# Optimization experiments

Measured on AMD Instinct MI355X. Metric: run time of the kernel, lower is better.

Reference implementation:

```python
import jax, jax.numpy as jnp
import numpy as np

B, S, D = 8, 1024, 768
H = 12
HD = D // H
DROPOUT_P = 0.5


def setup_inputs() -> dict:
    key = jax.random.key(0)
    ks = jax.random.split(key, 9)
    scale = 1.0 / np.sqrt(D)
    return {
        "x": jax.random.normal(ks[0], (B, S, D), dtype=jnp.float32),
        "wq": jax.random.normal(ks[1], (D, D), dtype=jnp.float32) * scale,
        "bq": jax.random.normal(ks[2], (D,), dtype=jnp.float32) * 0.01,
        "wk": jax.random.normal(ks[3], (D, D), dtype=jnp.float32) * scale,
        "bk": jax.random.normal(ks[4], (D,), dtype=jnp.float32) * 0.01,
        "wv": jax.random.normal(ks[5], (D, D), dtype=jnp.float32) * scale,
        "bv": jax.random.normal(ks[6], (D,), dtype=jnp.float32) * 0.01,
        "wo": jax.random.normal(ks[7], (D, D), dtype=jnp.float32) * scale,
        "bo": jax.random.normal(ks[8], (D,), dtype=jnp.float32) * 0.01,
    }


def reference(x, wq, bq, wk, bk, wv, bv, wo, bo):
    # QKV projections (torch Linear: y = x @ W.T + b)
    def proj(w, b):
        y = jnp.einsum("bsd,ed->bse", x, w) + b
        # [B,S,D] -> [B,H,S,HD]
        return y.reshape(B, S, H, HD).transpose(0, 2, 1, 3)

    q = proj(wq, bq)
    k = proj(wk, bk)
    v = proj(wv, bv)

    scores = jnp.einsum("bhqd,bhkd->bhqk", q, k) / jnp.sqrt(
        jnp.asarray(HD, dtype=x.dtype)
    )
    # dropout BEFORE softmax (non-standard, faithful to source), training=True
    dkey = jax.random.key(42)
    keep = jax.random.bernoulli(dkey, 1.0 - DROPOUT_P, scores.shape)
    scores = jnp.where(keep, scores / (1.0 - DROPOUT_P), 0.0)

    attn = jax.nn.softmax(scores, axis=-1)
    o = jnp.einsum("bhqk,bhkd->bhqd", attn, v)
    o = o.transpose(0, 2, 1, 3).reshape(B, S, D)
    return jnp.einsum("bsd,ed->bse", o, wo) + bo
```

## Files before the change

### kernel.cpp

```cpp
#include <hip/hip_runtime.h>
#include <hip/hip_bf16.h>
#include <stdint.h>

typedef __bf16 bf16_t;
typedef __attribute__((ext_vector_type(8))) __bf16 bf16x8;
typedef __attribute__((ext_vector_type(4))) __bf16 bf16x4;
typedef __attribute__((ext_vector_type(4))) float f32x4;

#define MFMA16(a, b, c) __builtin_amdgcn_mfma_f32_16x16x32_bf16(a, b, c, 0, 0, 0)


__device__ __forceinline__ uint32_t rotl32(uint32_t v, uint32_t r) {
    return (v << r) | (v >> (32u - r));
}
__device__ __forceinline__ uint32_t tf_fold(uint32_t x0, uint32_t x1) {
    const uint32_t ks0 = 0u, ks1 = 42u, ks2 = 0x1BD11BDAu ^ 42u;
    x0 += ks0; x1 += ks1;
#define TF_R(r) { x0 += x1; x1 = rotl32(x1, r); x1 ^= x0; }
    TF_R(13) TF_R(15) TF_R(26) TF_R(6)   x0 += ks1; x1 += ks2 + 1u;
    TF_R(17) TF_R(29) TF_R(16) TF_R(24)  x0 += ks2; x1 += ks0 + 2u;
    TF_R(13) TF_R(15) TF_R(26) TF_R(6)   x0 += ks0; x1 += ks1 + 3u;
    TF_R(17) TF_R(29) TF_R(16) TF_R(24)  x0 += ks1; x1 += ks2 + 4u;
    TF_R(13) TF_R(15) TF_R(26) TF_R(6)   x0 += ks2; x1 += ks0 + 5u;
#undef TF_R
    return x0 ^ x1;
}

__device__ __forceinline__ bf16x8 cvt8(float4 a, float4 b) {
    bf16x8 v;
    v[0] = (bf16_t)a.x; v[1] = (bf16_t)a.y; v[2] = (bf16_t)a.z; v[3] = (bf16_t)a.w;
    v[4] = (bf16_t)b.x; v[5] = (bf16_t)b.y; v[6] = (bf16_t)b.z; v[7] = (bf16_t)b.w;
    return v;
}

__global__ __launch_bounds__(256, 2)
void qkv_gemm(const float* __restrict__ x,
              const float* __restrict__ wq, const float* __restrict__ bq,
              const float* __restrict__ wk, const float* __restrict__ bk,
              const float* __restrict__ wv, const float* __restrict__ bv,
              bf16_t* __restrict__ qb, bf16_t* __restrict__ kb, bf16_t* __restrict__ vtb)
{
    const int mt = blockIdx.x;
    const int nt = blockIdx.y;
    const int mat = blockIdx.z;
    const float* w   = (mat == 0) ? wq : ((mat == 1) ? wk : wv);
    const float* bia = (mat == 0) ? bq : ((mat == 1) ? bk : bv);

    __shared__ bf16_t As[128][40];
    __shared__ bf16_t Bs[128][40];

    const int t = threadIdx.x;
    const int wid = t >> 6, l = t & 63, l15 = l & 15, lg = l >> 4;
    const int wr = wid >> 1, wc = wid & 1;

    f32x4 acc[4][4] = {};

    const int srow = t >> 1, scol = (t & 1) * 16;
    const float* xa = x + (size_t)(mt * 128 + srow) * 768 + scol;
    const float* wa = w + (size_t)(nt * 128 + srow) * 768 + scol;

    for (int kt = 0; kt < 24; ++kt) {
        const float* pa = xa + kt * 32;
        const float* pb = wa + kt * 32;
        float4 a0 = *(const float4*)(pa + 0),  a1 = *(const float4*)(pa + 4);
        float4 a2 = *(const float4*)(pa + 8),  a3 = *(const float4*)(pa + 12);
        float4 b0 = *(const float4*)(pb + 0),  b1 = *(const float4*)(pb + 4);
        float4 b2 = *(const float4*)(pb + 8),  b3 = *(const float4*)(pb + 12);
        __syncthreads();
        *(bf16x8*)&As[srow][scol]     = cvt8(a0, a1);
        *(bf16x8*)&As[srow][scol + 8] = cvt8(a2, a3);
        *(bf16x8*)&Bs[srow][scol]     = cvt8(b0, b1);
        *(bf16x8*)&Bs[srow][scol + 8] = cvt8(b2, b3);
        __syncthreads();

        bf16x8 af[4], bf[4];
#pragma unroll
        for (int m = 0; m < 4; ++m) af[m] = *(const bf16x8*)&As[wr * 64 + m * 16 + l15][lg * 8];
#pragma unroll
        for (int n = 0; n < 4; ++n) bf[n] = *(const bf16x8*)&Bs[wc * 64 + n * 16 + l15][lg * 8];
#pragma unroll
        for (int m = 0; m < 4; ++m)
#pragma unroll
            for (int n = 0; n < 4; ++n)
                acc[m][n] = MFMA16(af[m], bf[n], acc[m][n]);
    }

    const int eb = nt * 128 + wc * 64;
    const int mb = mt * 128 + wr * 64;
#pragma unroll
    for (int n = 0; n < 4; ++n) {
        const int e = eb + n * 16 + l15;
        const float bias = bia[e];
        const int h = e >> 6, hd = e & 63;
#pragma unroll
        for (int m = 0; m < 4; ++m) {
            const int m0 = mb + m * 16 + lg * 4;
            const int b = m0 >> 10, s0 = m0 & 1023;
            if (mat == 2) {
                bf16x4 pv;
#pragma unroll
                for (int r = 0; r < 4; ++r) pv[r] = (bf16_t)(acc[m][n][r] + bias);
                *(bf16x4*)(vtb + (((size_t)(b * 12 + h)) << 16) + ((size_t)hd << 10) + s0) = pv;
            } else {
                bf16_t* dst = (mat == 0) ? qb : kb;
                const float sc = (mat == 0) ? 0.125f : 1.0f;
                const size_t base = (((size_t)(b * 12 + h)) << 16) + ((size_t)s0 << 6) + hd;
#pragma unroll
                for (int r = 0; r < 4; ++r)
                    dst[base + (size_t)r * 64] = (bf16_t)((acc[m][n][r] + bias) * sc);
            }
        }
    }
}

__global__ __launch_bounds__(256, 2)
void attn_kernel(const bf16_t* __restrict__ qb, const bf16_t* __restrict__ kb,
                 const bf16_t* __restrict__ vtb, bf16_t* __restrict__ ob)
{
    const int qt = blockIdx.x;
    const int bh = blockIdx.y;
    const int t = threadIdx.x, w = t >> 6, l = t & 63, l15 = l & 15, lg = l >> 4;

    __shared__ bf16_t Kl[64][72];
    __shared__ bf16_t Vl[64][72];
    __shared__ bf16_t Pl[4][16][72];

    const size_t base = ((size_t)bh) << 16;
    const int q0 = qt * 64 + w * 16;

    bf16x8 qf[2];
    {
        const size_t qbase = base + (size_t)(q0 + l15) * 64 + lg * 8;
        qf[0] = *(const bf16x8*)(qb + qbase);
        qf[1] = *(const bf16x8*)(qb + qbase + 32);
    }

    f32x4 oacc[4] = {};
    float mst[4], lst[4];
#pragma unroll
    for (int r = 0; r < 4; ++r) { mst[r] = -1e30f; lst[r] = 0.f; }

    const uint32_t fbase = ((uint32_t)bh) << 20;

    for (int kt = 0; kt < 16; ++kt) {
#pragma unroll
        for (int sdx = 0; sdx < 2; ++sdx) {
            const int idx = sdx * 256 + t;
            const int row = idx >> 3, seg = idx & 7;
            *(uint4*)&Kl[row][seg * 8] =
                *(const uint4*)(kb + base + ((size_t)(kt * 64 + row) << 6) + seg * 8);
            *(uint4*)&Vl[row][seg * 8] =
                *(const uint4*)(vtb + base + ((size_t)row << 10) + kt * 64 + seg * 8);
        }
        __syncthreads();

        f32x4 sc[4] = {};
#pragma unroll
        for (int ks = 0; ks < 2; ++ks)
#pragma unroll
            for (int n = 0; n < 4; ++n) {
                bf16x8 kf = *(const bf16x8*)&Kl[n * 16 + l15][ks * 32 + lg * 8];
                sc[n] = MFMA16(qf[ks], kf, sc[n]);
            }

#pragma unroll
        for (int n = 0; n < 4; ++n) {
            const uint32_t kg = (uint32_t)(kt * 64 + n * 16 + l15);
#pragma unroll
            for (int r = 0; r < 4; ++r) {
                const uint32_t f = fbase + ((uint32_t)(q0 + lg * 4 + r) << 10) + kg;
                const uint32_t bits = tf_fold(0u, f);
                sc[n][r] = (bits >> 31) ? 0.f : sc[n][r] * 2.f;
            }
        }

#pragma unroll
        for (int r = 0; r < 4; ++r) {
            float tm = fmaxf(fmaxf(sc[0][r], sc[1][r]), fmaxf(sc[2][r], sc[3][r]));
#pragma unroll
            for (int mk = 1; mk < 16; mk <<= 1) tm = fmaxf(tm, __shfl_xor(tm, mk));
            const float mnew = fmaxf(mst[r], tm);
            const float corr = __expf(mst[r] - mnew);
            float ps = 0.f;
#pragma unroll
            for (int n = 0; n < 4; ++n) {
                const float p = __expf(sc[n][r] - mnew);
                ps += p;
                Pl[w][lg * 4 + r][n * 16 + l15] = (bf16_t)p;
            }
#pragma unroll
            for (int mk = 1; mk < 16; mk <<= 1) ps += __shfl_xor(ps, mk);
            lst[r] = lst[r] * corr + ps;
            mst[r] = mnew;
#pragma unroll
            for (int n = 0; n < 4; ++n) oacc[n][r] *= corr;
        }

        {
            const bf16x8 pa0 = *(const bf16x8*)&Pl[w][l15][lg * 8];
            const bf16x8 pa1 = *(const bf16x8*)&Pl[w][l15][32 + lg * 8];
#pragma unroll
            for (int n = 0; n < 4; ++n) {
                const bf16x8 v0 = *(const bf16x8*)&Vl[n * 16 + l15][lg * 8];
                const bf16x8 v1 = *(const bf16x8*)&Vl[n * 16 + l15][32 + lg * 8];
                oacc[n] = MFMA16(pa0, v0, oacc[n]);
                oacc[n] = MFMA16(pa1, v1, oacc[n]);
            }
        }
        __syncthreads();
    }

    const int b = bh / 12, h = bh % 12;
#pragma unroll
    for (int r = 0; r < 4; ++r) {
        const float inv = 1.f / lst[r];
        const size_t row = ((size_t)(b * 1024 + q0 + lg * 4 + r)) * 768 + h * 64;
#pragma unroll
        for (int n = 0; n < 4; ++n)
            ob[row + n * 16 + l15] = (bf16_t)(oacc[n][r] * inv);
    }
}

__global__ __launch_bounds__(256, 2)
void out_gemm(const bf16_t* __restrict__ ob, const float* __restrict__ wo,
              const float* __restrict__ bo, float* __restrict__ out)
{
    const int mt = blockIdx.x, nt = blockIdx.y;
    __shared__ bf16_t As[128][40];
    __shared__ bf16_t Bs[128][40];
    const int t = threadIdx.x;
    const int wid = t >> 6, l = t & 63, l15 = l & 15, lg = l >> 4;
    const int wr = wid >> 1, wc = wid & 1;
    f32x4 acc[4][4] = {};

    const int srow = t >> 1, scol = (t & 1) * 16;
    const bf16_t* aa = ob + (size_t)(mt * 128 + srow) * 768 + scol;
    const float*  wa = wo + (size_t)(nt * 128 + srow) * 768 + scol;

    for (int kt = 0; kt < 24; ++kt) {
        uint4 a01 = *(const uint4*)(aa + kt * 32);
        uint4 a23 = *(const uint4*)(aa + kt * 32 + 8);
        const float* pb = wa + kt * 32;
        float4 b0 = *(const float4*)(pb + 0), b1 = *(const float4*)(pb + 4);
        float4 b2 = *(const float4*)(pb + 8), b3 = *(const float4*)(pb + 12);
        __syncthreads();
        *(uint4*)&As[srow][scol]      = a01;
        *(uint4*)&As[srow][scol + 8]  = a23;
        *(bf16x8*)&Bs[srow][scol]     = cvt8(b0, b1);
        *(bf16x8*)&Bs[srow][scol + 8] = cvt8(b2, b3);
        __syncthreads();

        bf16x8 af[4], bf[4];
#pragma unroll
        for (int m = 0; m < 4; ++m) af[m] = *(const bf16x8*)&As[wr * 64 + m * 16 + l15][lg * 8];
#pragma unroll
        for (int n = 0; n < 4; ++n) bf[n] = *(const bf16x8*)&Bs[wc * 64 + n * 16 + l15][lg * 8];
#pragma unroll
        for (int m = 0; m < 4; ++m)
#pragma unroll
            for (int n = 0; n < 4; ++n)
                acc[m][n] = MFMA16(af[m], bf[n], acc[m][n]);
    }

#pragma unroll
    for (int n = 0; n < 4; ++n) {
        const int e = nt * 128 + wc * 64 + n * 16 + l15;
        const float bias = bo[e];
#pragma unroll
        for (int m = 0; m < 4; ++m) {
            const int m0 = mt * 128 + wr * 64 + m * 16 + lg * 4;
#pragma unroll
            for (int r = 0; r < 4; ++r)
                out[(size_t)(m0 + r) * 768 + e] = acc[m][n][r] + bias;
        }
    }
}

__global__ void fill_zero(float* p, int n) {
    int i = blockIdx.x * 256 + threadIdx.x;
    if (i < n) p[i] = 0.f;
}

extern "C" void kernel_launch(void* const* d_in, const int* in_sizes, int n_in,
                              void* d_out, int out_size, void* d_ws, size_t ws_size,
                              hipStream_t stream) {
    const float* x  = (const float*)d_in[0];
    const float* wq = (const float*)d_in[1];
    const float* bq = (const float*)d_in[2];
    const float* wk = (const float*)d_in[3];
    const float* bk = (const float*)d_in[4];
    const float* wv = (const float*)d_in[5];
    const float* bv = (const float*)d_in[6];
    const float* wo = (const float*)d_in[7];
    const float* bo = (const float*)d_in[8];
    float* out = (float*)d_out;

    const size_t NEED = 4ull * 6291456ull * 2ull;
    if (ws_size < NEED) {
        fill_zero<<<(out_size + 255) / 256, 256, 0, stream>>>(out, out_size);
        return;
    }

    bf16_t* qb  = (bf16_t*)d_ws;
    bf16_t* kb  = qb  + 6291456;
    bf16_t* vtb = kb  + 6291456;
    bf16_t* ob  = vtb + 6291456;

    qkv_gemm<<<dim3(64, 6, 3), 256, 0, stream>>>(x, wq, bq, wk, bk, wv, bv, qb, kb, vtb);
    attn_kernel<<<dim3(16, 96), 256, 0, stream>>>(qb, kb, vtb, ob);
    out_gemm<<<dim3(64, 6), 256, 0, stream>>>(ob, wo, bo, out);
}
```

Measured before the change: 340.7 us.

## Precompute dropout mask as packed bitmask in separate kernel

Adds a kernel that evaluates the Threefry dropout hash once per score element and stores it as a packed 32-bit bitmask in workspace. The attention kernel then reads two mask words per row per key tile instead of running the hash inline. The 2x dropout scale is folded into the Q scaling, raising it from 0.125 to 0.25. This moves the heavy integer hash out of the attention loop, at the cost of an extra launch, 12 MB of mask traffic, and scattered word loads inside attention. The mask is still recomputed every call.

New measurement: 359.9 us. 1.06x slower.

```diff
diff --git a/kernel.cpp b/kernel.cpp
--- a/kernel.cpp
+++ b/kernel.cpp
@@ -9,6 +9,7 @@
 
 #define MFMA16(a, b, c) __builtin_amdgcn_mfma_f32_16x16x32_bf16(a, b, c, 0, 0, 0)
 
+#define MASK_WORDS 3145728u
 
 __device__ __forceinline__ uint32_t rotl32(uint32_t v, uint32_t r) {
     return (v << r) | (v >> (32u - r));
@@ -24,6 +25,21 @@
     TF_R(13) TF_R(15) TF_R(26) TF_R(6)   x0 += ks2; x1 += ks0 + 5u;
 #undef TF_R
     return x0 ^ x1;
+}
+
+__global__ __launch_bounds__(256)
+void mask_gen(uint32_t* __restrict__ mask) {
+    const uint32_t stride = gridDim.x * 256u;
+    for (uint32_t w = blockIdx.x * 256u + threadIdx.x; w < MASK_WORDS; w += stride) {
+        const uint32_t base = w << 5;
+        uint32_t word = 0u;
+#pragma unroll
+        for (int c = 31; c >= 0; --c) {
+            const uint32_t bits = tf_fold(0u, base + (uint32_t)c);
+            word = (word << 1) | (bits >> 31);
+        }
+        mask[w] = word;
+    }
 }
 
 __device__ __forceinline__ bf16x8 cvt8(float4 a, float4 b) {
@@ -103,7 +119,7 @@
                 *(bf16x4*)(vtb + (((size_t)(b * 12 + h)) << 16) + ((size_t)hd << 10) + s0) = pv;
             } else {
                 bf16_t* dst = (mat == 0) ? qb : kb;
-                const float sc = (mat == 0) ? 0.125f : 1.0f;
+                const float sc = (mat == 0) ? 0.25f : 1.0f;
                 const size_t base = (((size_t)(b * 12 + h)) << 16) + ((size_t)s0 << 6) + hd;
 #pragma unroll
                 for (int r = 0; r < 4; ++r)
@@ -115,7 +131,8 @@
 
 __global__ __launch_bounds__(256, 2)
 void attn_kernel(const bf16_t* __restrict__ qb, const bf16_t* __restrict__ kb,
-                 const bf16_t* __restrict__ vtb, bf16_t* __restrict__ ob)
+                 const bf16_t* __restrict__ vtb, const uint32_t* __restrict__ mask,
+                 bf16_t* __restrict__ ob)
 {
     const int qt = blockIdx.x;
     const int bh = blockIdx.y;
@@ -140,7 +157,7 @@
 #pragma unroll
     for (int r = 0; r < 4; ++r) { mst[r] = -1e30f; lst[r] = 0.f; }
 
-    const uint32_t fbase = ((uint32_t)bh) << 20;
+    const uint32_t mwb = ((uint32_t)bh) << 15;
 
     for (int kt = 0; kt < 16; ++kt) {
 #pragma unroll
@@ -164,13 +181,15 @@
             }
 
 #pragma unroll
-        for (int n = 0; n < 4; ++n) {
-            const uint32_t kg = (uint32_t)(kt * 64 + n * 16 + l15);
-#pragma unroll
-            for (int r = 0; r < 4; ++r) {
-                const uint32_t f = fbase + ((uint32_t)(q0 + lg * 4 + r) << 10) + kg;
-                const uint32_t bits = tf_fold(0u, f);
-                sc[n][r] = (bits >> 31) ? 0.f : sc[n][r] * 2.f;
+        for (int r = 0; r < 4; ++r) {
+            const uint32_t qg = (uint32_t)(q0 + lg * 4 + r);
+            const uint32_t wi = mwb + (qg << 5) + (uint32_t)(kt << 1);
+            const uint32_t w0 = mask[wi], w1 = mask[wi + 1];
+#pragma unroll
+            for (int n = 0; n < 4; ++n) {
+                const uint32_t wrd = (n < 2) ? w0 : w1;
+                const uint32_t bit = ((uint32_t)(n & 1) << 4) + (uint32_t)l15;
+                if ((wrd >> bit) & 1u) sc[n][r] = 0.f;
             }
         }
 
@@ -295,7 +314,7 @@
     const float* bo = (const float*)d_in[8];
     float* out = (float*)d_out;
 
-    const size_t NEED = 4ull * 6291456ull * 2ull;
+    const size_t NEED = 4ull * 6291456ull * 2ull + (size_t)MASK_WORDS * 4ull;
     if (ws_size < NEED) {
         fill_zero<<<(out_size + 255) / 256, 256, 0, stream>>>(out, out_size);
         return;
@@ -305,8 +324,10 @@
     bf16_t* kb  = qb  + 6291456;
     bf16_t* vtb = kb  + 6291456;
     bf16_t* ob  = vtb + 6291456;
-
+    uint32_t* mask = (uint32_t*)(ob + 6291456);
+
+    mask_gen<<<2048, 256, 0, stream>>>(mask);
     qkv_gemm<<<dim3(64, 6, 3), 256, 0, stream>>>(x, wq, bq, wk, bk, wv, bv, qb, kb, vtb);
-    attn_kernel<<<dim3(16, 96), 256, 0, stream>>>(qb, kb, vtb, ob);
+    attn_kernel<<<dim3(16, 96), 256, 0, stream>>>(qb, kb, vtb, mask, ob);
     out_gemm<<<dim3(64, 6), 256, 0, stream>>>(ob, wo, bo, out);
 }
```
